# Performance work log

Hardware: AMD Instinct MI355X
Metric: run time of the kernel (lower is better)

Reference implementation:

```python
import jax, jax.numpy as jnp
import numpy as np

GRID = 2
SPAN = 2.0
EMBED = 64
HIDDEN = 128
PRED_LEN = 12
N = 1024
T = 8
SCENE_SIZE = 64


def _social_pool(ht, pos, scene, active):
    """ht: [N,H], pos: [N,2], scene: [N] int, active: [N] bool -> [N, GRID*GRID, H].
    Vectorized equivalent of the per-scene scatter_add pooling: pairwise mask over
    same-scene, active, within-area, non-self pairs; bin neighbor hidden states."""
    n = ht.shape[0]
    half = SPAN / 2.0
    eps = 0.01
    rel = pos[None, :, :] - pos[:, None, :]  # rel[i,j] = pos_j - pos_i
    within = ((rel[..., 0] < half - eps) & (rel[..., 0] > -half + eps)
              & (rel[..., 1] < half - eps) & (rel[..., 1] > -half + eps))
    pair = (within & (~jnp.eye(n, dtype=bool))
            & (scene[:, None] == scene[None, :])
            & active[:, None] & active[None, :])
    cell = SPAN / GRID
    gidx = jnp.floor((rel + half) / cell).astype(jnp.int32)
    gid = jnp.clip(gidx[..., 0] * GRID + gidx[..., 1], 0, GRID * GRID - 1)
    onehot = jax.nn.one_hot(gid, GRID * GRID, dtype=ht.dtype) * pair[..., None].astype(ht.dtype)
    # pooled[i,g,h] = sum_j onehot[i,j,g] * ht[j,h]
    return jnp.einsum('ijg,jh->igh', onehot, ht)


def _lstm_step(x, h, c, Wih, Whh, bih, bhh):
    z = x @ Wih.T + bih + h @ Whh.T + bhh
    i, f, g, o = jnp.split(z, 4, axis=-1)
    c_new = jax.nn.sigmoid(f) * c + jax.nn.sigmoid(i) * jnp.tanh(g)
    h_new = jax.nn.sigmoid(o) * jnp.tanh(c_new)
    return h_new, c_new


def setup_inputs() -> dict:
    key = jax.random.key(0)
    ks = jax.random.split(key, 16)
    past_traj = jax.random.uniform(ks[0], (N, T, 2), dtype=jnp.float32) * 8.0
    past_traj_rel = jax.random.normal(ks[1], (N, T, 2), dtype=jnp.float32)
    past_traj_timestamp_mask = jnp.ones((N, T), dtype=jnp.int32)
    is_predictable = jnp.ones((N, 1), dtype=jnp.int32)
    same_scene_mask = (jnp.arange(N, dtype=jnp.int32) // SCENE_SIZE).reshape(N, 1)

    def lin(k, fan_out, fan_in):
        b = 1.0 / np.sqrt(fan_in)
        return jax.random.uniform(k, (fan_out, fan_in), jnp.float32, -b, b)

    pos_W = lin(ks[2], EMBED, 2)
    pos_b = jnp.zeros((EMBED,), jnp.float32)
    soc_W = lin(ks[3], EMBED, GRID * GRID * HIDDEN)
    soc_b = jnp.zeros((EMBED,), jnp.float32)
    Wih = lin(ks[4], 4 * HIDDEN, 2 * EMBED)
    Whh = lin(ks[5], 4 * HIDDEN, HIDDEN)
    bih = jnp.zeros((4 * HIDDEN,), jnp.float32)
    bhh = jnp.zeros((4 * HIDDEN,), jnp.float32)
    h0 = jax.random.normal(ks[6], (HIDDEN,), jnp.float32) * 0.1
    c0 = jax.random.normal(ks[7], (HIDDEN,), jnp.float32) * 0.1
    pred_W = lin(ks[8], 5, HIDDEN)
    pred_b = jnp.zeros((5,), jnp.float32)
    return {
        'past_traj': past_traj, 'past_traj_rel': past_traj_rel,
        'past_traj_timestamp_mask': past_traj_timestamp_mask,
        'is_predictable': is_predictable, 'same_scene_mask': same_scene_mask,
        'pos_W': pos_W, 'pos_b': pos_b, 'soc_W': soc_W, 'soc_b': soc_b,
        'Wih': Wih, 'Whh': Whh, 'bih': bih, 'bhh': bhh,
        'h0': h0, 'c0': c0, 'pred_W': pred_W, 'pred_b': pred_b,
    }


def reference(past_traj, past_traj_rel, past_traj_timestamp_mask, is_predictable,
              same_scene_mask, pos_W, pos_b, soc_W, soc_b, Wih, Whh, bih, bhh,
              h0, c0, pred_W, pred_b):
    n = past_traj.shape[0]
    scene = same_scene_mask[:, 0]
    ht = jnp.broadcast_to(h0[None, :], (n, HIDDEN))
    ct = jnp.broadcast_to(c0[None, :], (n, HIDDEN))

    def obs_step(carry, inp):
        ht, ct = carry
        point, rel, m = inp  # [N,2], [N,2], [N]
        active = m == 1
        pooled = _social_pool(ht, point, scene, active)  # [N,G^2,H]
        et = jax.nn.relu(rel @ pos_W.T + pos_b)
        at = jax.nn.relu(pooled.reshape(n, -1) @ soc_W.T + soc_b)
        x = jnp.concatenate([et, at], axis=-1)
        h_new, c_new = _lstm_step(x, ht, ct, Wih, Whh, bih, bhh)
        ht = jnp.where(active[:, None], h_new, ht)
        ct = jnp.where(active[:, None], c_new, ct)
        return (ht, ct), None

    obs_inp = (jnp.moveaxis(past_traj, 1, 0), jnp.moveaxis(past_traj_rel, 1, 0),
               jnp.moveaxis(past_traj_timestamp_mask, 1, 0))
    (ht, ct), _ = jax.lax.scan(obs_step, (ht, ct), obs_inp)

    pred_active = past_traj_timestamp_mask[:, -1] == 1
    pos0 = past_traj[:, -1, :]

    def pred_step(carry, _):
        ht, ct, pos = carry
        out = ht @ pred_W.T + pred_b  # [N,5]
        rel = out[:, :2]
        pos = pos + rel
        pooled = _social_pool(ht, pos, scene, pred_active)
        et = jax.nn.relu(rel @ pos_W.T + pos_b)
        at = jax.nn.relu(pooled.reshape(n, -1) @ soc_W.T + soc_b)
        x = jnp.concatenate([et, at], axis=-1)
        h_new, c_new = _lstm_step(x, ht, ct, Wih, Whh, bih, bhh)
        ht = jnp.where(pred_active[:, None], h_new, ht)
        ct = jnp.where(pred_active[:, None], c_new, ct)
        return (ht, ct, pos), (out, pos)

    (_, _, _), (outs, trajs) = jax.lax.scan(pred_step, (ht, ct, pos0), None, length=PRED_LEN)
    pred_out_all = jnp.where(pred_active[:, None, None], jnp.moveaxis(outs, 0, 1), 0.0)
    pred_traj_all = jnp.where(pred_active[:, None, None], jnp.moveaxis(trajs, 0, 1), 0.0)
    # is_predictable is all-ones in this setup, so the final boolean filter is identity
    return pred_out_all, pred_traj_all
```

## Files before the change

### kernel.cpp

```cpp
#include <hip/hip_runtime.h>

#define NAGENT 64
#define HID    128
#define TOBS   8
#define PREDL  12
#define NTHR   1024
#define XP     264
#define PP     264
#define S2P    264

typedef __attribute__((ext_vector_type(8))) short bf16x8;
typedef __attribute__((ext_vector_type(4))) short bf16x4;
typedef __attribute__((ext_vector_type(4))) float f32x4;

__device__ __forceinline__ unsigned short f2bf(float f) {
    unsigned int x = __float_as_uint(f);
    unsigned int r = (x + 0x7fffu + ((x >> 16) & 1u)) >> 16;
    return (unsigned short)r;
}
__device__ __forceinline__ float bf2f(unsigned short u) {
    return __uint_as_float(((unsigned int)u) << 16);
}
__device__ __forceinline__ float sigmf(float x) {
    return __builtin_amdgcn_rcpf(1.0f + __expf(-x));
}
__device__ __forceinline__ float tanhf_fast(float x) {
    x = fminf(fmaxf(x, -15.0f), 15.0f);
    float e = __expf(2.0f * x);
    return (e - 1.0f) * __builtin_amdgcn_rcpf(e + 1.0f);
}
__device__ __forceinline__ float sel4(float a0, float a1, float a2, float a3, int k) {
    float lo = (k & 1) ? a1 : a0;
    float hi = (k & 1) ? a3 : a2;
    return (k & 2) ? hi : lo;
}

__global__ void prep_weights(const float* __restrict__ Wih, const float* __restrict__ Whh,
                             const float* __restrict__ socW,
                             unsigned short* __restrict__ wd, unsigned short* __restrict__ wb) {
    int idx = blockIdx.x * blockDim.x + threadIdx.x;
    if (idx < 131072) {
        int e = idx & 7, l = (idx >> 3) & 63, t = idx >> 9;
        int kt = t & 7, nt = t >> 3;
        int k = kt * 32 + ((l >> 4) << 3) + e;
        int n = nt * 16 + (l & 15);
        int d = n >> 2, g = n & 3;
        int row = g * 128 + d;
        float v = (k < 128) ? Wih[row * 128 + k] : Whh[row * 128 + (k - 128)];
        wd[idx] = f2bf(v);
    } else if (idx < 163840) {
        int idx2 = idx - 131072;
        int e = idx2 & 7, l = (idx2 >> 3) & 63, t = idx2 >> 9;
        int kt = t & 3, nt = t >> 2;
        int k = kt * 32 + ((l >> 4) << 3) + e;
        int r = nt * 16 + (l & 15);
        int eo = r >> 2, g = r & 3;
        wb[idx2] = f2bf(socW[eo * 512 + g * 128 + k]);
    }
}

__global__ __launch_bounds__(NTHR) void social_lstm_mfma(
    const float* __restrict__ past_traj, const float* __restrict__ past_traj_rel,
    const int* __restrict__ ts_mask, const int* __restrict__ scene_in,
    const float* __restrict__ pos_W, const float* __restrict__ pos_b,
    const float* __restrict__ soc_b,
    const float* __restrict__ bih, const float* __restrict__ bhh,
    const float* __restrict__ h0, const float* __restrict__ c0,
    const float* __restrict__ pred_W, const float* __restrict__ pred_b,
    const unsigned short* __restrict__ wd, const unsigned short* __restrict__ wb,
    float* __restrict__ out)
{
    __shared__ __align__(16) unsigned short sh_X[NAGENT][XP];
    __shared__ __align__(16) unsigned short sh_P[NAGENT][PP];
    __shared__ __align__(16) unsigned short sh_S2[NAGENT][S2P];
    __shared__ float sh_px[NAGENT], sh_py[NAGENT], sh_rx[NAGENT], sh_ry[NAGENT];
    __shared__ float sh_o[5][NAGENT];
    __shared__ int   sh_act[NAGENT], sh_scene[NAGENT];

    const int tid  = threadIdx.x;
    const int lane = tid & 63;
    const int wv   = __builtin_amdgcn_readfirstlane(tid >> 6);
    const int gbase = blockIdx.x * NAGENT;
    const int c16 = lane & 15;
    const int q4  = lane >> 4;
    const int go  = c16 & 3;
    const int dq  = c16 >> 2;

    float bs[2], c_st[4][2], hnew[4][2];
    int dimv[2];
    #pragma unroll
    for (int s = 0; s < 2; ++s) {
        const int n = (2 * wv + s) * 16 + c16;
        const int d = n >> 2, g = n & 3;
        bs[s] = bih[g * 128 + d] + bhh[g * 128 + d];
        dimv[s] = (2 * wv + s) * 4 + dq;
        #pragma unroll
        for (int mj = 0; mj < 4; ++mj) c_st[mj][s] = c0[dimv[s]];
    }
    for (int p = tid; p < NAGENT * HID; p += NTHR) {
        int a = p >> 7, d = p & 127;
        sh_X[a][128 + d] = f2bf(h0[d]);
    }
    if (tid < NAGENT) sh_scene[tid] = scene_in[gbase + tid];
    __syncthreads();

    const bf16x8* wdp = (const bf16x8*)wd + (2 * wv * 8) * 64 + lane;
    const bf16x8* wbp = (const bf16x8*)wb + (wv * 4) * 64 + lane;
    const unsigned short* xaD = &sh_X[c16][q4 * 8];
    const unsigned short* xaB = &sh_X[c16][128 + q4 * 8];

    for (int step = 0; step < TOBS + PREDL; ++step) {
        if (step < TOBS) {
            if (tid < NAGENT) {
                const int ig = gbase + tid;
                sh_px[tid] = past_traj[(ig * TOBS + step) * 2 + 0];
                sh_py[tid] = past_traj[(ig * TOBS + step) * 2 + 1];
                sh_rx[tid] = past_traj_rel[(ig * TOBS + step) * 2 + 0];
                sh_ry[tid] = past_traj_rel[(ig * TOBS + step) * 2 + 1];
                sh_act[tid] = (ts_mask[ig * TOBS + step] == 1) ? 1 : 0;
            }
        } else {
            if (tid < 5 * NAGENT) {
                float acc = pred_b[wv];
                const float* pw = pred_W + wv * HID;
                #pragma unroll
                for (int u = 0; u < 16; ++u) {
                    const bf16x8 v = *(const bf16x8*)&sh_X[lane][128 + u * 8];
                    #pragma unroll
                    for (int e = 0; e < 8; ++e)
                        acc += bf2f((unsigned short)v[e]) * pw[u * 8 + e];
                }
                sh_o[wv][lane] = acc;
            }
            __syncthreads();
            if (tid < NAGENT) {
                const int i = tid;
                const float rx = sh_o[0][i], ry = sh_o[1][i];
                const float px = sh_px[i] + rx, py = sh_py[i] + ry;
                sh_px[i] = px; sh_py[i] = py;
                sh_rx[i] = rx; sh_ry[i] = ry;
                const float m = sh_act[i] ? 1.0f : 0.0f;
                const int p = step - TOBS;
                const int ig = gbase + i;
                float* po = out + (ig * PREDL + p) * 5;
                #pragma unroll
                for (int q = 0; q < 5; ++q) po[q] = m * sh_o[q][i];
                float* pt = out + 61440 + (ig * PREDL + p) * 2;
                pt[0] = m * px; pt[1] = m * py;
            }
        }
        __syncthreads();

        #pragma unroll
        for (int it = 0; it < 4; ++it) {
            const int p = (it << 10) + tid;
            const int i = p >> 6, j = p & 63;
            const float dx = sh_px[j] - sh_px[i];
            const float dy = sh_py[j] - sh_py[i];
            const bool within = (dx < 0.99f) & (dx > -0.99f) & (dy < 0.99f) & (dy > -0.99f);
            const bool pair = within && (i != j) && (sh_scene[i] == sh_scene[j])
                              && sh_act[i] && sh_act[j];
            int gid = (int)floorf(dx + 1.0f) * 2 + (int)floorf(dy + 1.0f);
            gid = min(max(gid, 0), 3);
            #pragma unroll
            for (int g = 0; g < 4; ++g)
                sh_P[i][g * 64 + j] = (pair && gid == g) ? (unsigned short)0x3f80
                                                         : (unsigned short)0;
        }
        {
            const float rx = sh_rx[lane], ry = sh_ry[lane];
            const int e0 = wv * 4;
            #pragma unroll
            for (int u = 0; u < 4; ++u) {
                const int e = e0 + u;
                sh_X[lane][e] = f2bf(fmaxf(pos_b[e] + rx * pos_W[e * 2] + ry * pos_W[e * 2 + 1], 0.f));
            }
        }
        {
            f32x4 acc2[4];
            #pragma unroll
            for (int mj = 0; mj < 4; ++mj) acc2[mj] = (f32x4){0.f, 0.f, 0.f, 0.f};
            #pragma unroll
            for (int kt = 0; kt < 4; ++kt) {
                const bf16x8 b = wbp[kt * 64];
                #pragma unroll
                for (int mj = 0; mj < 4; ++mj) {
                    const bf16x8 a = *(const bf16x8*)(xaB + mj * 16 * XP + kt * 32);
                    acc2[mj] = __builtin_amdgcn_mfma_f32_16x16x32_bf16(a, b, acc2[mj], 0, 0, 0);
                }
            }
            const int r = wv * 16 + c16;
            unsigned short* dst = &sh_S2[r >> 2][(r & 3) * 64 + q4 * 4];
            #pragma unroll
            for (int mj = 0; mj < 4; ++mj) {
                bf16x4 pk;
                #pragma unroll
                for (int i = 0; i < 4; ++i) pk[i] = (short)f2bf(acc2[mj][i]);
                *(bf16x4*)(dst + mj * 16) = pk;
            }
        }
        __syncthreads();

        {
            const int mt = wv & 3, nt = wv >> 2;
            f32x4 acc = (f32x4){0.f, 0.f, 0.f, 0.f};
            const unsigned short* pa = &sh_P[mt * 16 + c16][q4 * 8];
            const unsigned short* pb = &sh_S2[nt * 16 + c16][q4 * 8];
            #pragma unroll
            for (int kt = 0; kt < 8; ++kt) {
                const bf16x8 a = *(const bf16x8*)(pa + kt * 32);
                const bf16x8 b = *(const bf16x8*)(pb + kt * 32);
                acc = __builtin_amdgcn_mfma_f32_16x16x32_bf16(a, b, acc, 0, 0, 0);
            }
            const int e_ = nt * 16 + c16;
            const float sb = soc_b[e_];
            #pragma unroll
            for (int rr = 0; rr < 4; ++rr)
                sh_X[mt * 16 + q4 * 4 + rr][64 + e_] = f2bf(fmaxf(acc[rr] + sb, 0.f));
        }
        __syncthreads();

        {
            f32x4 acc[4][2];
            #pragma unroll
            for (int mj = 0; mj < 4; ++mj) {
                acc[mj][0] = (f32x4){0.f, 0.f, 0.f, 0.f};
                acc[mj][1] = (f32x4){0.f, 0.f, 0.f, 0.f};
            }
            #pragma unroll 2
            for (int kt = 0; kt < 8; ++kt) {
                const bf16x8 b0 = wdp[kt * 64];
                const bf16x8 b1 = wdp[kt * 64 + 512];
                #pragma unroll
                for (int mj = 0; mj < 4; ++mj) {
                    const bf16x8 a = *(const bf16x8*)(xaD + mj * 16 * XP + kt * 32);
                    acc[mj][0] = __builtin_amdgcn_mfma_f32_16x16x32_bf16(a, b0, acc[mj][0], 0, 0, 0);
                    acc[mj][1] = __builtin_amdgcn_mfma_f32_16x16x32_bf16(a, b1, acc[mj][1], 0, 0, 0);
                }
            }
            #pragma unroll
            for (int mj = 0; mj < 4; ++mj) {
                const int a = mj * 16 + q4 * 4 + go;
                const bool act = sh_act[a] != 0;
                #pragma unroll
                for (int s = 0; s < 2; ++s) {
                    const float z0 = acc[mj][s][0] + bs[s];
                    const float z1 = acc[mj][s][1] + bs[s];
                    const float z2 = acc[mj][s][2] + bs[s];
                    const float z3 = acc[mj][s][3] + bs[s];
                    const float s0 = sel4(z0, z1, z2, z3, go);
                    const float s1 = sel4(z0, z1, z2, z3, go ^ 1);
                    const float s2 = sel4(z0, z1, z2, z3, go ^ 2);
                    const float s3 = sel4(z0, z1, z2, z3, go ^ 3);
                    const float t1 = __shfl_xor(s1, 1, 64);
                    const float t2 = __shfl_xor(s2, 2, 64);
                    const float t3 = __shfl_xor(s3, 3, 64);
                    const float zi = sel4(s0, t1, t2, t3, go);
                    const float zf = sel4(s0, t1, t2, t3, go ^ 1);
                    const float zg = sel4(s0, t1, t2, t3, go ^ 2);
                    const float zo = sel4(s0, t1, t2, t3, go ^ 3);
                    const float cold = c_st[mj][s];
                    const float cn = sigmf(zf) * cold + sigmf(zi) * tanhf_fast(zg);
                    const float hn = sigmf(zo) * tanhf_fast(cn);
                    c_st[mj][s] = act ? cn : cold;
                    const float hold = bf2f(sh_X[a][128 + dimv[s]]);
                    hnew[mj][s] = act ? hn : hold;
                }
            }
        }
        __syncthreads();
        #pragma unroll
        for (int mj = 0; mj < 4; ++mj) {
            const int a = mj * 16 + q4 * 4 + go;
            sh_X[a][128 + dimv[0]] = f2bf(hnew[mj][0]);
            sh_X[a][128 + dimv[1]] = f2bf(hnew[mj][1]);
        }
        __syncthreads();
    }
}

extern "C" void kernel_launch(void* const* d_in, const int* in_sizes, int n_in,
                              void* d_out, int out_size, void* d_ws, size_t ws_size,
                              hipStream_t stream) {
    (void)in_sizes; (void)n_in; (void)out_size; (void)ws_size;
    unsigned short* wd = (unsigned short*)d_ws;
    unsigned short* wb = wd + 131072;
    prep_weights<<<640, 256, 0, stream>>>(
        (const float*)d_in[9], (const float*)d_in[10], (const float*)d_in[7], wd, wb);
    social_lstm_mfma<<<16, NTHR, 0, stream>>>(
        (const float*)d_in[0],
        (const float*)d_in[1],
        (const int*)  d_in[2],
        (const int*)  d_in[4],
        (const float*)d_in[5],
        (const float*)d_in[6],
        (const float*)d_in[8],
        (const float*)d_in[11],
        (const float*)d_in[12],
        (const float*)d_in[13],
        (const float*)d_in[14],
        (const float*)d_in[15],
        (const float*)d_in[16],
        wd, wb,
        (float*)d_out);
}
```

Baseline: 294.1 us.

## Use MFMA for prediction head and interleave pooling mask layout

The per-agent prediction head, previously a scalar dot product over 5 waves, now runs as MFMA on 4 waves. Its weights are split into bf16 hi and lo parts so the result stays close to fp32. The pairwise pooling mask is re-laid out with the grid index interleaved per neighbour, so each thread writes one 8-byte store instead of four scalar stores, and the grid-cell computation is simplified to sign tests. The intermediate social-weight product is stored in row-major form, and its B operand is assembled from two 4-element loads. This trades scattered scalar LDS stores in the S writeback for cheaper mask writes and less serial head work.

```diff
diff --git a/kernel.cpp b/kernel.cpp
--- a/kernel.cpp
+++ b/kernel.cpp
@@ -7,11 +7,12 @@
 #define NTHR   1024
 #define XP     264
 #define PP     264
-#define S2P    264
+#define SP2    264
 
 typedef __attribute__((ext_vector_type(8))) short bf16x8;
 typedef __attribute__((ext_vector_type(4))) short bf16x4;
 typedef __attribute__((ext_vector_type(4))) float f32x4;
+typedef __attribute__((ext_vector_type(2))) unsigned int u32x2;
 
 __device__ __forceinline__ unsigned short f2bf(float f) {
     unsigned int x = __float_as_uint(f);
@@ -36,9 +37,10 @@
 }
 
 __global__ void prep_weights(const float* __restrict__ Wih, const float* __restrict__ Whh,
-                             const float* __restrict__ socW,
-                             unsigned short* __restrict__ wd, unsigned short* __restrict__ wb) {
-    int idx = blockIdx.x * blockDim.x + threadIdx.x;
+                             const float* __restrict__ socW, const float* __restrict__ predW,
+                             unsigned short* __restrict__ wd, unsigned short* __restrict__ wb,
+                             unsigned short* __restrict__ wp) {
+    int idx = blockIdx.x * 256 + threadIdx.x;
     if (idx < 131072) {
         int e = idx & 7, l = (idx >> 3) & 63, t = idx >> 9;
         int kt = t & 7, nt = t >> 3;
@@ -49,13 +51,22 @@
         float v = (k < 128) ? Wih[row * 128 + k] : Whh[row * 128 + (k - 128)];
         wd[idx] = f2bf(v);
     } else if (idx < 163840) {
-        int idx2 = idx - 131072;
-        int e = idx2 & 7, l = (idx2 >> 3) & 63, t = idx2 >> 9;
+        int i2 = idx - 131072;
+        int e = i2 & 7, l = (i2 >> 3) & 63, t = i2 >> 9;
         int kt = t & 3, nt = t >> 2;
         int k = kt * 32 + ((l >> 4) << 3) + e;
         int r = nt * 16 + (l & 15);
         int eo = r >> 2, g = r & 3;
-        wb[idx2] = f2bf(socW[eo * 512 + g * 128 + k]);
+        wb[i2] = f2bf(socW[eo * 512 + g * 128 + k]);
+    } else if (idx < 167936) {
+        int i3 = idx - 163840;
+        int e = i3 & 7, l = (i3 >> 3) & 63, f = i3 >> 9;
+        int kt = f & 3, half = f >> 2;
+        int k = kt * 32 + ((l >> 4) << 3) + e;
+        int n = l & 15;
+        float v = (n < 5) ? predW[n * 128 + k] : 0.0f;
+        unsigned short hi = f2bf(v);
+        wp[i3] = half ? f2bf(v - bf2f(hi)) : hi;
     }
 }
 
@@ -66,13 +77,14 @@
     const float* __restrict__ soc_b,
     const float* __restrict__ bih, const float* __restrict__ bhh,
     const float* __restrict__ h0, const float* __restrict__ c0,
-    const float* __restrict__ pred_W, const float* __restrict__ pred_b,
+    const float* __restrict__ pred_b,
     const unsigned short* __restrict__ wd, const unsigned short* __restrict__ wb,
+    const unsigned short* __restrict__ wp,
     float* __restrict__ out)
 {
     __shared__ __align__(16) unsigned short sh_X[NAGENT][XP];
     __shared__ __align__(16) unsigned short sh_P[NAGENT][PP];
-    __shared__ __align__(16) unsigned short sh_S2[NAGENT][S2P];
+    __shared__ __align__(16) unsigned short sh_S[NAGENT][SP2];
     __shared__ float sh_px[NAGENT], sh_py[NAGENT], sh_rx[NAGENT], sh_ry[NAGENT];
     __shared__ float sh_o[5][NAGENT];
     __shared__ int   sh_act[NAGENT], sh_scene[NAGENT];
@@ -120,17 +132,21 @@
                 sh_act[tid] = (ts_mask[ig * TOBS + step] == 1) ? 1 : 0;
             }
         } else {
-            if (tid < 5 * NAGENT) {
-                float acc = pred_b[wv];
-                const float* pw = pred_W + wv * HID;
-                #pragma unroll
-                for (int u = 0; u < 16; ++u) {
-                    const bf16x8 v = *(const bf16x8*)&sh_X[lane][128 + u * 8];
+            if (wv < 4) {
+                const bf16x8* wpv = (const bf16x8*)wp;
+                f32x4 pa = (f32x4){0.f, 0.f, 0.f, 0.f};
+                #pragma unroll
+                for (int kt = 0; kt < 4; ++kt) {
+                    const bf16x8 a = *(const bf16x8*)&sh_X[wv * 16 + c16][128 + kt * 32 + q4 * 8];
+                    pa = __builtin_amdgcn_mfma_f32_16x16x32_bf16(a, wpv[kt * 64 + lane], pa, 0, 0, 0);
+                    pa = __builtin_amdgcn_mfma_f32_16x16x32_bf16(a, wpv[(4 + kt) * 64 + lane], pa, 0, 0, 0);
+                }
+                if (c16 < 5) {
+                    const float pb = pred_b[c16];
                     #pragma unroll
-                    for (int e = 0; e < 8; ++e)
-                        acc += bf2f((unsigned short)v[e]) * pw[u * 8 + e];
-                }
-                sh_o[wv][lane] = acc;
+                    for (int rr = 0; rr < 4; ++rr)
+                        sh_o[c16][wv * 16 + q4 * 4 + rr] = pa[rr] + pb;
+                }
             }
             __syncthreads();
             if (tid < NAGENT) {
@@ -153,19 +169,23 @@
 
         #pragma unroll
         for (int it = 0; it < 4; ++it) {
-            const int p = (it << 10) + tid;
+            const int p = it * NTHR + tid;
             const int i = p >> 6, j = p & 63;
             const float dx = sh_px[j] - sh_px[i];
             const float dy = sh_py[j] - sh_py[i];
             const bool within = (dx < 0.99f) & (dx > -0.99f) & (dy < 0.99f) & (dy > -0.99f);
             const bool pair = within && (i != j) && (sh_scene[i] == sh_scene[j])
                               && sh_act[i] && sh_act[j];
-            int gid = (int)floorf(dx + 1.0f) * 2 + (int)floorf(dy + 1.0f);
-            gid = min(max(gid, 0), 3);
-            #pragma unroll
-            for (int g = 0; g < 4; ++g)
-                sh_P[i][g * 64 + j] = (pair && gid == g) ? (unsigned short)0x3f80
-                                                         : (unsigned short)0;
+            const int gid = ((dx >= 0.f) ? 2 : 0) + ((dy >= 0.f) ? 1 : 0);
+            unsigned int w0 = 0, w1 = 0;
+            if (pair) {
+                if (gid == 0) w0 = 0x3f80u;
+                else if (gid == 1) w0 = 0x3f800000u;
+                else if (gid == 2) w1 = 0x3f80u;
+                else w1 = 0x3f800000u;
+            }
+            u32x2 w; w[0] = w0; w[1] = w1;
+            *(u32x2*)&sh_P[i][j * 4] = w;
         }
         {
             const float rx = sh_rx[lane], ry = sh_ry[lane];
@@ -189,34 +209,33 @@
                     acc2[mj] = __builtin_amdgcn_mfma_f32_16x16x32_bf16(a, b, acc2[mj], 0, 0, 0);
                 }
             }
-            const int r = wv * 16 + c16;
-            unsigned short* dst = &sh_S2[r >> 2][(r & 3) * 64 + q4 * 4];
-            #pragma unroll
-            for (int mj = 0; mj < 4; ++mj) {
-                bf16x4 pk;
-                #pragma unroll
-                for (int i = 0; i < 4; ++i) pk[i] = (short)f2bf(acc2[mj][i]);
-                *(bf16x4*)(dst + mj * 16) = pk;
-            }
+            const int rcol = wv * 16 + c16;
+            #pragma unroll
+            for (int mj = 0; mj < 4; ++mj)
+                #pragma unroll
+                for (int rr = 0; rr < 4; ++rr)
+                    sh_S[mj * 16 + q4 * 4 + rr][rcol] = f2bf(acc2[mj][rr]);
         }
         __syncthreads();
 
         {
             const int mt = wv & 3, nt = wv >> 2;
-            f32x4 acc = (f32x4){0.f, 0.f, 0.f, 0.f};
-            const unsigned short* pa = &sh_P[mt * 16 + c16][q4 * 8];
-            const unsigned short* pb = &sh_S2[nt * 16 + c16][q4 * 8];
+            const int cb = 4 * (nt * 16 + c16);
+            f32x4 cac = (f32x4){0.f, 0.f, 0.f, 0.f};
             #pragma unroll
             for (int kt = 0; kt < 8; ++kt) {
-                const bf16x8 a = *(const bf16x8*)(pa + kt * 32);
-                const bf16x8 b = *(const bf16x8*)(pb + kt * 32);
-                acc = __builtin_amdgcn_mfma_f32_16x16x32_bf16(a, b, acc, 0, 0, 0);
-            }
-            const int e_ = nt * 16 + c16;
-            const float sb = soc_b[e_];
+                const bf16x8 a = *(const bf16x8*)&sh_P[mt * 16 + c16][kt * 32 + q4 * 8];
+                const int j0 = kt * 8 + q4 * 2;
+                const bf16x4 lo = *(const bf16x4*)&sh_S[j0][cb];
+                const bf16x4 hi = *(const bf16x4*)&sh_S[j0 + 1][cb];
+                const bf16x8 b = __builtin_shufflevector(lo, hi, 0, 1, 2, 3, 4, 5, 6, 7);
+                cac = __builtin_amdgcn_mfma_f32_16x16x32_bf16(a, b, cac, 0, 0, 0);
+            }
+            const int e = nt * 16 + c16;
+            const float sb = soc_b[e];
             #pragma unroll
             for (int rr = 0; rr < 4; ++rr)
-                sh_X[mt * 16 + q4 * 4 + rr][64 + e_] = f2bf(fmaxf(acc[rr] + sb, 0.f));
+                sh_X[mt * 16 + q4 * 4 + rr][64 + e] = f2bf(fmaxf(cac[rr] + sb, 0.f));
         }
         __syncthreads();
 
@@ -285,8 +304,10 @@
     (void)in_sizes; (void)n_in; (void)out_size; (void)ws_size;
     unsigned short* wd = (unsigned short*)d_ws;
     unsigned short* wb = wd + 131072;
-    prep_weights<<<640, 256, 0, stream>>>(
-        (const float*)d_in[9], (const float*)d_in[10], (const float*)d_in[7], wd, wb);
+    unsigned short* wp = wb + 32768;
+    prep_weights<<<656, 256, 0, stream>>>(
+        (const float*)d_in[9], (const float*)d_in[10],
+        (const float*)d_in[7], (const float*)d_in[15], wd, wb, wp);
     social_lstm_mfma<<<16, NTHR, 0, stream>>>(
         (const float*)d_in[0],
         (const float*)d_in[1],
@@ -299,8 +320,7 @@
         (const float*)d_in[12],
         (const float*)d_in[13],
         (const float*)d_in[14],
-        (const float*)d_in[15],
         (const float*)d_in[16],
-        wd, wb,
+        wd, wb, wp,
         (float*)d_out);
 }
```

Result: no change. 290.2 us (-1.3%).
